# Performance work log

Hardware: AMD Instinct MI355X
Metric: run time of the kernel (lower is better)

## Reference

```python
import jax, jax.numpy as jnp
import numpy as np
from jax import lax

BN_EPS = 1e-5


def setup_inputs() -> dict:
    key = jax.random.key(0)
    ks = jax.random.split(key, 7)
    B, Cin, H, W = 16, 256, 80, 80
    Cout, K = 512, 3
    x = jax.random.normal(ks[0], (B, Cin, H, W), dtype=jnp.float32)
    # grouped-conv kernel: OIHW with I = in_per_group = 1, feature_group_count = Cin
    w = jax.random.normal(ks[1], (Cout, 1, K, K), dtype=jnp.float32) * 0.1
    b = jax.random.normal(ks[2], (Cout,), dtype=jnp.float32) * 0.1
    bn_gamma = jax.random.uniform(ks[3], (Cout,), dtype=jnp.float32, minval=0.5, maxval=1.5)
    bn_beta = jax.random.normal(ks[4], (Cout,), dtype=jnp.float32) * 0.1
    bn_mean = jax.random.normal(ks[5], (Cout,), dtype=jnp.float32) * 0.1
    bn_var = jax.random.uniform(ks[6], (Cout,), dtype=jnp.float32, minval=0.5, maxval=1.5)
    return {"x": x, "w": w, "b": b, "bn_gamma": bn_gamma, "bn_beta": bn_beta,
            "bn_mean": bn_mean, "bn_var": bn_var}


def reference(x, w, b, bn_gamma, bn_beta, bn_mean, bn_var):
    # The torch module's loop over `group` Conv2d(in_per_group, out_per_group)
    # blocks + concat is exactly one grouped conv with feature_group_count=group.
    groups = x.shape[1] // w.shape[1]
    pad = (w.shape[2] - 1) // 2
    y = lax.conv_general_dilated(
        x, w,
        window_strides=(1, 1),
        padding=((pad, pad), (pad, pad)),
        dimension_numbers=("NCHW", "OIHW", "NCHW"),
        feature_group_count=groups,
    )
    y = y + b[None, :, None, None]
    # per-channel BatchNorm (inference form) -- per-group BN params concatenated
    inv = bn_gamma * lax.rsqrt(bn_var + BN_EPS)
    y = y * inv[None, :, None, None] + (bn_beta - bn_mean * inv)[None, :, None, None]
    # SiLU
    return y * jax.nn.sigmoid(y)
```

## Files before the change

### kernel.cpp

```cpp
#include <hip/hip_runtime.h>
#include <math.h>


#define CS_B    16
#define CS_CIN  256
#define CS_COUT 512
#define CS_H    80
#define CS_W    80
#define CS_HP   82
#define CS_WS   84
#define BN_EPS  1e-5f
#define NQ      (CS_H * CS_W / 4)
#define QPR     (CS_W / 4)

__global__ __launch_bounds__(256) void csconv_kernel(
    const float* __restrict__ x,
    const float* __restrict__ wgt,
    const float* __restrict__ bias,
    const float* __restrict__ gamma,
    const float* __restrict__ beta,
    const float* __restrict__ mean,
    const float* __restrict__ var,
    float* __restrict__ out)
{
    const int blk = blockIdx.x;
    const int g   = blk & (CS_CIN - 1);
    const int b   = blk >> 8;
    const int tid = threadIdx.x;

    __shared__ float tile[CS_HP][CS_WS];

    {
        float4 z4 = make_float4(0.f, 0.f, 0.f, 0.f);
        float4* t4 = (float4*)&tile[0][0];
        for (int i = tid; i < CS_HP * CS_WS / 4; i += 256) t4[i] = z4;
    }
    __syncthreads();

    const float* xp = x + (size_t)(b * CS_CIN + g) * (CS_H * CS_W);
    const float4* xp4 = (const float4*)xp;
    for (int q = tid; q < NQ; q += 256) {
        int r  = q / QPR;
        int c4 = (q - r * QPR) * 4;
        float4 v = xp4[q];
        tile[r + 1][c4 + 1] = v.x;
        tile[r + 1][c4 + 2] = v.y;
        tile[r + 1][c4 + 3] = v.z;
        tile[r + 1][c4 + 4] = v.w;
    }
    __syncthreads();

    const int co0 = 2 * g;
    const int co1 = co0 + 1;

    float k0[9], k1[9];
#pragma unroll
    for (int t = 0; t < 9; ++t) {
        k0[t] = wgt[co0 * 9 + t];
        k1[t] = wgt[co1 * 9 + t];
    }
    const float s0 = gamma[co0] * rsqrtf(var[co0] + BN_EPS);
    const float s1 = gamma[co1] * rsqrtf(var[co1] + BN_EPS);
    const float t0 = beta[co0] + (bias[co0] - mean[co0]) * s0;
    const float t1 = beta[co1] + (bias[co1] - mean[co1]) * s1;

    float* op0 = out + ((size_t)b * CS_COUT + co0) * (CS_H * CS_W);
    float* op1 = op0 + CS_H * CS_W;

    for (int q = tid; q < NQ; q += 256) {
        int r  = q / QPR;
        int c4 = (q - r * QPR) * 4;

        float acc0[4] = {0.f, 0.f, 0.f, 0.f};
        float acc1[4] = {0.f, 0.f, 0.f, 0.f};
#pragma unroll
        for (int kh = 0; kh < 3; ++kh) {
            float4 va = *(const float4*)&tile[r + kh][c4];
            float2 vb = *(const float2*)&tile[r + kh][c4 + 4];
            float v0 = va.x, v1 = va.y, v2 = va.z, v3 = va.w;
            float v4 = vb.x, v5 = vb.y;
            float w00 = k0[kh * 3 + 0], w01 = k0[kh * 3 + 1], w02 = k0[kh * 3 + 2];
            float w10 = k1[kh * 3 + 0], w11 = k1[kh * 3 + 1], w12 = k1[kh * 3 + 2];
            acc0[0] = fmaf(v0, w00, fmaf(v1, w01, fmaf(v2, w02, acc0[0])));
            acc0[1] = fmaf(v1, w00, fmaf(v2, w01, fmaf(v3, w02, acc0[1])));
            acc0[2] = fmaf(v2, w00, fmaf(v3, w01, fmaf(v4, w02, acc0[2])));
            acc0[3] = fmaf(v3, w00, fmaf(v4, w01, fmaf(v5, w02, acc0[3])));
            acc1[0] = fmaf(v0, w10, fmaf(v1, w11, fmaf(v2, w12, acc1[0])));
            acc1[1] = fmaf(v1, w10, fmaf(v2, w11, fmaf(v3, w12, acc1[1])));
            acc1[2] = fmaf(v2, w10, fmaf(v3, w11, fmaf(v4, w12, acc1[2])));
            acc1[3] = fmaf(v3, w10, fmaf(v4, w11, fmaf(v5, w12, acc1[3])));
        }

        float4 y0, y1;
        float* y0p = &y0.x;
        float* y1p = &y1.x;
#pragma unroll
        for (int j = 0; j < 4; ++j) {
            float a0 = fmaf(acc0[j], s0, t0);
            float a1 = fmaf(acc1[j], s1, t1);
            y0p[j] = __fdividef(a0, 1.0f + __expf(-a0));
            y1p[j] = __fdividef(a1, 1.0f + __expf(-a1));
        }
        ((float4*)op0)[q] = y0;
        ((float4*)op1)[q] = y1;
    }
}

extern "C" void kernel_launch(void* const* d_in, const int* in_sizes, int n_in,
                              void* d_out, int out_size, void* d_ws, size_t ws_size,
                              hipStream_t stream) {
    const float* x     = (const float*)d_in[0];
    const float* wgt   = (const float*)d_in[1];
    const float* bias  = (const float*)d_in[2];
    const float* gamma = (const float*)d_in[3];
    const float* beta  = (const float*)d_in[4];
    const float* mean  = (const float*)d_in[5];
    const float* var   = (const float*)d_in[6];
    float* out = (float*)d_out;

    dim3 grid(CS_B * CS_CIN);
    dim3 block(256);
    csconv_kernel<<<grid, block, 0, stream>>>(x, wgt, bias, gamma, beta, mean, var, out);
}
```

Measured before the change: 303.3 us.

## Drop shared-memory tile and read 3x3 halo directly from global memory

Removes the zero-filled padded LDS tile and its two barriers. Each thread now loads its three rows (a float4 plus left and right scalars) straight from global memory and applies the zero padding with predicates. The block size goes from 256 to 320 so that the 1600 quads per plane divide evenly into five iterations. Overlapping rows are re-read through the cache instead of from LDS, which adds global load traffic but cuts barrier stalls and LDS occupancy limits.

Measured after the change: 322.3 us. +6.3%, slower.

```diff
diff --git a/kernel.cpp b/kernel.cpp
--- a/kernel.cpp
+++ b/kernel.cpp
@@ -7,13 +7,12 @@
 #define CS_COUT 512
 #define CS_H    80
 #define CS_W    80
-#define CS_HP   82
-#define CS_WS   84
 #define BN_EPS  1e-5f
 #define NQ      (CS_H * CS_W / 4)
 #define QPR     (CS_W / 4)
+#define THREADS 320
 
-__global__ __launch_bounds__(256) void csconv_kernel(
+__global__ __launch_bounds__(THREADS) void csconv_kernel(
     const float* __restrict__ x,
     const float* __restrict__ wgt,
     const float* __restrict__ bias,
@@ -23,32 +22,11 @@
     const float* __restrict__ var,
     float* __restrict__ out)
 {
-    const int blk = blockIdx.x;
-    const int g   = blk & (CS_CIN - 1);
-    const int b   = blk >> 8;
-    const int tid = threadIdx.x;
+    const int plane = blockIdx.x;
+    const int g     = plane & (CS_CIN - 1);
+    const int tid   = threadIdx.x;
 
-    __shared__ float tile[CS_HP][CS_WS];
-
-    {
-        float4 z4 = make_float4(0.f, 0.f, 0.f, 0.f);
-        float4* t4 = (float4*)&tile[0][0];
-        for (int i = tid; i < CS_HP * CS_WS / 4; i += 256) t4[i] = z4;
-    }
-    __syncthreads();
-
-    const float* xp = x + (size_t)(b * CS_CIN + g) * (CS_H * CS_W);
-    const float4* xp4 = (const float4*)xp;
-    for (int q = tid; q < NQ; q += 256) {
-        int r  = q / QPR;
-        int c4 = (q - r * QPR) * 4;
-        float4 v = xp4[q];
-        tile[r + 1][c4 + 1] = v.x;
-        tile[r + 1][c4 + 2] = v.y;
-        tile[r + 1][c4 + 3] = v.z;
-        tile[r + 1][c4 + 4] = v.w;
-    }
-    __syncthreads();
+    const float* xp = x + (size_t)plane * (CS_H * CS_W);
 
     const int co0 = 2 * g;
     const int co1 = co0 + 1;
@@ -64,31 +42,46 @@
     const float t0 = beta[co0] + (bias[co0] - mean[co0]) * s0;
     const float t1 = beta[co1] + (bias[co1] - mean[co1]) * s1;
 
-    float* op0 = out + ((size_t)b * CS_COUT + co0) * (CS_H * CS_W);
+    float* op0 = out + (size_t)(2 * plane) * (CS_H * CS_W);
     float* op1 = op0 + CS_H * CS_W;
 
-    for (int q = tid; q < NQ; q += 256) {
-        int r  = q / QPR;
-        int c4 = (q - r * QPR) * 4;
+    for (int q = tid; q < NQ; q += THREADS) {
+        const int r  = q / QPR;
+        const int c4 = (q - r * QPR) * 4;
+
+        const float* rm = xp + r * CS_W;
+        const float* rt = (r > 0)          ? rm - CS_W : rm;
+        const float* rb = (r < CS_H - 1)   ? rm + CS_W : rm;
+        const int cl = (c4 > 0)            ? c4 - 1 : 0;
+        const int cr = (c4 < CS_W - 4)     ? c4 + 4 : CS_W - 1;
+
+        float4 m0 = *(const float4*)&rt[c4]; float l0 = rt[cl]; float r0 = rt[cr];
+        float4 m1 = *(const float4*)&rm[c4]; float l1 = rm[cl]; float r1 = rm[cr];
+        float4 m2 = *(const float4*)&rb[c4]; float l2 = rb[cl]; float r2 = rb[cr];
+
+        const bool mt = (r > 0), mb = (r < CS_H - 1), ml = (c4 > 0), mr = (c4 < CS_W - 4);
+        if (!mt) { m0 = make_float4(0.f, 0.f, 0.f, 0.f); l0 = 0.f; r0 = 0.f; }
+        if (!mb) { m2 = make_float4(0.f, 0.f, 0.f, 0.f); l2 = 0.f; r2 = 0.f; }
+        l0 = ml ? l0 : 0.f; l1 = ml ? l1 : 0.f; l2 = ml ? l2 : 0.f;
+        r0 = mr ? r0 : 0.f; r1 = mr ? r1 : 0.f; r2 = mr ? r2 : 0.f;
+
+        float v[3][6] = {
+            { l0, m0.x, m0.y, m0.z, m0.w, r0 },
+            { l1, m1.x, m1.y, m1.z, m1.w, r1 },
+            { l2, m2.x, m2.y, m2.z, m2.w, r2 },
+        };
 
         float acc0[4] = {0.f, 0.f, 0.f, 0.f};
         float acc1[4] = {0.f, 0.f, 0.f, 0.f};
 #pragma unroll
         for (int kh = 0; kh < 3; ++kh) {
-            float4 va = *(const float4*)&tile[r + kh][c4];
-            float2 vb = *(const float2*)&tile[r + kh][c4 + 4];
-            float v0 = va.x, v1 = va.y, v2 = va.z, v3 = va.w;
-            float v4 = vb.x, v5 = vb.y;
             float w00 = k0[kh * 3 + 0], w01 = k0[kh * 3 + 1], w02 = k0[kh * 3 + 2];
             float w10 = k1[kh * 3 + 0], w11 = k1[kh * 3 + 1], w12 = k1[kh * 3 + 2];
-            acc0[0] = fmaf(v0, w00, fmaf(v1, w01, fmaf(v2, w02, acc0[0])));
-            acc0[1] = fmaf(v1, w00, fmaf(v2, w01, fmaf(v3, w02, acc0[1])));
-            acc0[2] = fmaf(v2, w00, fmaf(v3, w01, fmaf(v4, w02, acc0[2])));
-            acc0[3] = fmaf(v3, w00, fmaf(v4, w01, fmaf(v5, w02, acc0[3])));
-            acc1[0] = fmaf(v0, w10, fmaf(v1, w11, fmaf(v2, w12, acc1[0])));
-            acc1[1] = fmaf(v1, w10, fmaf(v2, w11, fmaf(v3, w12, acc1[1])));
-            acc1[2] = fmaf(v2, w10, fmaf(v3, w11, fmaf(v4, w12, acc1[2])));
-            acc1[3] = fmaf(v3, w10, fmaf(v4, w11, fmaf(v5, w12, acc1[3])));
+#pragma unroll
+            for (int j = 0; j < 4; ++j) {
+                acc0[j] = fmaf(v[kh][j], w00, fmaf(v[kh][j+1], w01, fmaf(v[kh][j+2], w02, acc0[j])));
+                acc1[j] = fmaf(v[kh][j], w10, fmaf(v[kh][j+1], w11, fmaf(v[kh][j+2], w12, acc1[j])));
+            }
         }
 
         float4 y0, y1;
@@ -119,6 +112,6 @@
     float* out = (float*)d_out;
 
     dim3 grid(CS_B * CS_CIN);
-    dim3 block(256);
+    dim3 block(THREADS);
     csconv_kernel<<<grid, block, 0, stream>>>(x, wgt, bias, gamma, beta, mean, var, out);
 }
```
